# Optimization experiments

Hardware: AMD Instinct MI355X
Metric: run time of the kernel (lower is better)

The kernel has to match this reference:

```python
import jax, jax.numpy as jnp
import numpy as np

INPUT_DIM = 1024
HIDDEN_DIM = 1024

def setup_inputs() -> dict:
    key = jax.random.key(0)
    ks = jax.random.split(key, 9)
    s_in = 1.0 / np.sqrt(INPUT_DIM)
    s_h = 1.0 / np.sqrt(HIDDEN_DIM)
    x = jax.random.normal(ks[0], (4, 2048, INPUT_DIM), dtype=jnp.float32)
    Wq = jax.random.uniform(ks[1], (INPUT_DIM, HIDDEN_DIM), jnp.float32, -s_in, s_in)
    bq = jax.random.uniform(ks[2], (HIDDEN_DIM,), jnp.float32, -s_in, s_in)
    Wk = jax.random.uniform(ks[3], (INPUT_DIM, HIDDEN_DIM), jnp.float32, -s_in, s_in)
    bk = jax.random.uniform(ks[4], (HIDDEN_DIM,), jnp.float32, -s_in, s_in)
    Wv = jax.random.uniform(ks[5], (INPUT_DIM, HIDDEN_DIM), jnp.float32, -s_in, s_in)
    bv = jax.random.uniform(ks[6], (HIDDEN_DIM,), jnp.float32, -s_in, s_in)
    Wo = jax.random.uniform(ks[7], (HIDDEN_DIM, INPUT_DIM), jnp.float32, -s_h, s_h)
    bo = jax.random.uniform(ks[8], (INPUT_DIM,), jnp.float32, -s_h, s_h)
    return {"x": x, "Wq": Wq, "bq": bq, "Wk": Wk, "bk": bk, "Wv": Wv, "bv": bv, "Wo": Wo, "bo": bo}

def reference(x, Wq, bq, Wk, bk, Wv, bv, Wo, bo):
    # x: [B, S, D_in]; scale uses x.shape[-1] (faithful to source, which divides by sqrt(input_dim))
    scale = 1.0 / jnp.sqrt(jnp.asarray(x.shape[-1], dtype=x.dtype))
    Q = jnp.einsum('bsd,dh->bsh', x, Wq) + bq
    K = jnp.einsum('bsd,dh->bsh', x, Wk) + bk
    V = jnp.einsum('bsd,dh->bsh', x, Wv) + bv
    scores = jnp.einsum('bqh,bkh->bqk', Q, K) * scale  # [B, S, S]
    attn = jax.nn.softmax(scores, axis=-1)
    ctx = jnp.einsum('bqk,bkh->bqh', attn, V)
    return jnp.einsum('bsh,hd->bsd', ctx, Wo) + bo
```

## Files before the change

kernel.cpp:

```cpp
#include <hip/hip_runtime.h>

typedef __attribute__((ext_vector_type(8))) short bf16x8;
typedef __attribute__((ext_vector_type(4))) float f32x4;
typedef __attribute__((ext_vector_type(4))) unsigned short us4;

#define AS1 __attribute__((address_space(1)))
#define AS3 __attribute__((address_space(3)))

__device__ __forceinline__ unsigned short f2bf(float f) {
  unsigned u = __float_as_uint(f);
  u += 0x7fff + ((u >> 16) & 1);
  return (unsigned short)(u >> 16);
}

__device__ __forceinline__ void gload_lds16(const void* g, void* l) {
  __builtin_amdgcn_global_load_lds((const AS1 unsigned int*)g,
                                   (AS3 unsigned int*)l, 16, 0, 0);
}

#define MFMA16(a, b, c) __builtin_amdgcn_mfma_f32_16x16x32_bf16(a, b, c, 0, 0, 0)

template <typename OutT, bool BIAS, int MODE>
__global__ __launch_bounds__(512, 2) void gemm8p(
    const unsigned short* __restrict__ A,
    const unsigned short* __restrict__ Bt,
    OutT* __restrict__ C,
    unsigned short* __restrict__ Vt,
    const float* __restrict__ bias,
    int Kd, int lda, int ldb, int ldc,
    long sA, long sB, long sC,
    float scale) {
  constexpr int BOFF = 256 * 64;
  __shared__ unsigned short lds[2][512 * 64];

  const int bz = blockIdx.z;
  A  += (size_t)bz * sA + (size_t)blockIdx.x * 256 * lda;
  Bt += (size_t)bz * sB + (size_t)blockIdx.y * 256 * ldb;

  const int tid  = threadIdx.x;
  const int wave = tid >> 6;
  const int lane = tid & 63;
  const int wm   = wave >> 2;
  const int wn   = wave & 3;
  const int l15  = lane & 15;
  const int hi   = lane >> 4;
  const int sr  = (wave << 3) + (lane >> 3);
  const int sc8 = lane & 7;
  const int co0 = ((hi    ) ^ (lane & 7)) << 3;
  const int co1 = ((hi + 4) ^ (lane & 7)) << 3;
  const int rA0 = wm * 128 + l15;
  const int rB0 = wn * 32 + l15;

  auto stA = [&](int b, int k0, int r0) {
    const unsigned short* g =
        A + (size_t)(r0 + sr) * lda + (k0 + ((sc8 ^ (sr & 7)) << 3));
    gload_lds16(g, &lds[b][(r0 + (wave << 3)) * 64]);
  };
  auto stB = [&](int b, int k0, int r0) {
    const int lr = r0 + sr;
    const int gr = ((lr >> 5) & 3) * 64 + ((lr >> 7) << 5) + (lr & 31);
    const unsigned short* g =
        Bt + (size_t)gr * ldb + (k0 + ((sc8 ^ (lr & 7)) << 3));
    gload_lds16(g, &lds[b][BOFF + (r0 + (wave << 3)) * 64]);
  };

  f32x4 acc[8][4] = {};
  bf16x8 af[4][2], b0f[2][2], b1f[2][2];

  stA(0, 0, 0);   stA(0, 0, 128);
  stB(0, 0, 0);   stB(0, 0, 64);
  stB(0, 0, 128); stB(0, 0, 192);
  stA(0, 0, 64);  stA(0, 0, 192);
  asm volatile("s_waitcnt vmcnt(4)" ::: "memory");
  __builtin_amdgcn_s_barrier();

  const int NT = Kd >> 6;
  for (int t = 0; t < NT; ++t) {
    const int buf = t & 1;
    const int nb  = buf ^ 1;
    const int nk0 = (t + 1) << 6;
    const bool st = (t + 1) < NT;
    const unsigned short* Lr = &lds[buf][0];

#pragma unroll
    for (int mt = 0; mt < 4; ++mt) {
      af[mt][0] = *(const bf16x8*)&Lr[(rA0 + mt * 16) * 64 + co0];
      af[mt][1] = *(const bf16x8*)&Lr[(rA0 + mt * 16) * 64 + co1];
    }
#pragma unroll
    for (int n = 0; n < 2; ++n) {
      b0f[n][0] = *(const bf16x8*)&Lr[BOFF + (rB0 + n * 16) * 64 + co0];
      b0f[n][1] = *(const bf16x8*)&Lr[BOFF + (rB0 + n * 16) * 64 + co1];
    }
    if (st) { stA(nb, nk0, 0); stA(nb, nk0, 128); stB(nb, nk0, 0); stB(nb, nk0, 64); }
    __builtin_amdgcn_s_barrier();
    __builtin_amdgcn_s_setprio(1);
#pragma unroll
    for (int mt = 0; mt < 4; ++mt)
#pragma unroll
      for (int n = 0; n < 2; ++n) {
        acc[mt][n] = MFMA16(af[mt][0], b0f[n][0], acc[mt][n]);
        acc[mt][n] = MFMA16(af[mt][1], b0f[n][1], acc[mt][n]);
      }
    __builtin_amdgcn_s_setprio(0);
    if (st) asm volatile("s_waitcnt vmcnt(4)" ::: "memory");
    else    asm volatile("s_waitcnt vmcnt(0)" ::: "memory");
    __builtin_amdgcn_s_barrier();

#pragma unroll
    for (int n = 0; n < 2; ++n) {
      b1f[n][0] = *(const bf16x8*)&Lr[BOFF + (128 + rB0 + n * 16) * 64 + co0];
      b1f[n][1] = *(const bf16x8*)&Lr[BOFF + (128 + rB0 + n * 16) * 64 + co1];
    }
    if (st) { stB(nb, nk0, 128); stB(nb, nk0, 192); stA(nb, nk0, 64); stA(nb, nk0, 192); }
    __builtin_amdgcn_s_barrier();
    __builtin_amdgcn_s_setprio(1);
#pragma unroll
    for (int mt = 0; mt < 4; ++mt)
#pragma unroll
      for (int n = 0; n < 2; ++n) {
        acc[mt][2 + n] = MFMA16(af[mt][0], b1f[n][0], acc[mt][2 + n]);
        acc[mt][2 + n] = MFMA16(af[mt][1], b1f[n][1], acc[mt][2 + n]);
      }
    __builtin_amdgcn_s_setprio(0);
    __builtin_amdgcn_s_barrier();

#pragma unroll
    for (int mt = 0; mt < 4; ++mt) {
      af[mt][0] = *(const bf16x8*)&Lr[(64 + rA0 + mt * 16) * 64 + co0];
      af[mt][1] = *(const bf16x8*)&Lr[(64 + rA0 + mt * 16) * 64 + co1];
    }
    __builtin_amdgcn_s_barrier();
    __builtin_amdgcn_s_setprio(1);
#pragma unroll
    for (int mt = 0; mt < 4; ++mt)
#pragma unroll
      for (int n = 0; n < 2; ++n) {
        acc[4 + mt][2 + n] = MFMA16(af[mt][0], b1f[n][0], acc[4 + mt][2 + n]);
        acc[4 + mt][2 + n] = MFMA16(af[mt][1], b1f[n][1], acc[4 + mt][2 + n]);
      }
    __builtin_amdgcn_s_setprio(0);
    __builtin_amdgcn_s_barrier();

    __builtin_amdgcn_s_barrier();
    __builtin_amdgcn_s_setprio(1);
#pragma unroll
    for (int mt = 0; mt < 4; ++mt)
#pragma unroll
      for (int n = 0; n < 2; ++n) {
        acc[4 + mt][n] = MFMA16(af[mt][0], b0f[n][0], acc[4 + mt][n]);
        acc[4 + mt][n] = MFMA16(af[mt][1], b0f[n][1], acc[4 + mt][n]);
      }
    __builtin_amdgcn_s_setprio(0);
    if (st) asm volatile("s_waitcnt vmcnt(4)" ::: "memory");
    __builtin_amdgcn_s_barrier();
  }

  const int hi4  = hi << 2;
  const int row0 = blockIdx.x * 256 + wm * 128;
  const int col0 = blockIdx.y * 256 + wn * 64;

  if constexpr (MODE == 1) {
    const int piece = col0 >> 10;
    float bvv[4];
#pragma unroll
    for (int nt = 0; nt < 4; ++nt)
      bvv[nt] = BIAS ? bias[col0 + nt * 16 + l15] : 0.0f;
    if (piece < 2) {
      OutT* dst = C + (size_t)piece * sC;
      const int cb = (col0 & 1023) + l15;
#pragma unroll
      for (int mt = 0; mt < 8; ++mt)
#pragma unroll
        for (int r = 0; r < 4; ++r) {
          const size_t rowoff = (size_t)(row0 + mt * 16 + hi4 + r) * ldc;
#pragma unroll
          for (int nt = 0; nt < 4; ++nt)
            dst[rowoff + cb + nt * 16] = (OutT)f2bf(acc[mt][nt][r] * scale + bvv[nt]);
        }
    } else {
      const int b = blockIdx.x >> 3;
      const int sb = (blockIdx.x & 7) * 256 + wm * 128 + hi4;
#pragma unroll
      for (int nt = 0; nt < 4; ++nt) {
        const int d = ((col0 + nt * 16) & 1023) + l15;
#pragma unroll
        for (int mt = 0; mt < 8; ++mt) {
          us4 pk;
          pk.x = f2bf(acc[mt][nt][0] * scale + bvv[nt]);
          pk.y = f2bf(acc[mt][nt][1] * scale + bvv[nt]);
          pk.z = f2bf(acc[mt][nt][2] * scale + bvv[nt]);
          pk.w = f2bf(acc[mt][nt][3] * scale + bvv[nt]);
          *(us4*)&Vt[((size_t)b << 21) + (size_t)d * 2048 + sb + mt * 16] = pk;
        }
      }
    }
  } else {
    C += (size_t)bz * sC;
    float bvv[4];
#pragma unroll
    for (int nt = 0; nt < 4; ++nt)
      bvv[nt] = BIAS ? bias[col0 + nt * 16 + l15] : 0.0f;
    const int cb = col0 + l15;
#pragma unroll
    for (int mt = 0; mt < 8; ++mt)
#pragma unroll
      for (int r = 0; r < 4; ++r) {
        const size_t rowoff = (size_t)(row0 + mt * 16 + hi4 + r) * ldc;
#pragma unroll
        for (int nt = 0; nt < 4; ++nt) {
          const float v = acc[mt][nt][r] * scale + bvv[nt];
          if constexpr (sizeof(OutT) == 4)
            C[rowoff + cb + nt * 16] = v;
          else
            C[rowoff + cb + nt * 16] = (OutT)f2bf(v);
        }
      }
  }
}

__global__ void cvt_x(const float* __restrict__ in, unsigned short* __restrict__ out, int n4) {
  const int i = blockIdx.x * blockDim.x + threadIdx.x;
  if (i < n4) {
    const float4 v = ((const float4*)in)[i];
    uint2 o;
    o.x = (unsigned)f2bf(v.x) | ((unsigned)f2bf(v.y) << 16);
    o.y = (unsigned)f2bf(v.z) | ((unsigned)f2bf(v.w) << 16);
    ((uint2*)out)[i] = o;
  }
}

__global__ void cvtT_w4(const float* __restrict__ Wq, const float* __restrict__ Wk,
                        const float* __restrict__ Wv, const float* __restrict__ Wo,
                        unsigned short* __restrict__ Wqkvb, unsigned short* __restrict__ Wob) {
  __shared__ unsigned short tile[64][65];
  const int z = blockIdx.z;
  const float* in = (z == 0) ? Wq : (z == 1) ? Wk : (z == 2) ? Wv : Wo;
  unsigned short* out = (z == 3) ? Wob : Wqkvb + (size_t)z * 1024 * 1024;
  const int r0 = blockIdx.y * 64, c0 = blockIdx.x * 64;
  for (int i = threadIdx.y; i < 64; i += 4)
    tile[i][threadIdx.x] = f2bf(in[(size_t)(r0 + i) * 1024 + c0 + threadIdx.x]);
  __syncthreads();
  for (int i = threadIdx.y; i < 64; i += 4)
    out[(size_t)(c0 + i) * 1024 + r0 + threadIdx.x] = tile[threadIdx.x][i];
}

__global__ void concat_bias(const float* __restrict__ bq, const float* __restrict__ bk,
                            const float* __restrict__ bv, float* __restrict__ dst) {
  const int z = blockIdx.x;
  const float* src = (z == 0) ? bq : (z == 1) ? bk : bv;
  const int i = threadIdx.x;
  ((float4*)(dst + z * 1024))[i] = ((const float4*)src)[i];
}

__global__ __launch_bounds__(256) void softmax_bf16(unsigned short* __restrict__ scores) {
  unsigned short* p = scores + (size_t)blockIdx.x * 2048;
  const int t = threadIdx.x;
  uint4 raw = ((const uint4*)p)[t];
  float v[8];
  v[0] = __uint_as_float(raw.x << 16); v[1] = __uint_as_float(raw.x & 0xffff0000u);
  v[2] = __uint_as_float(raw.y << 16); v[3] = __uint_as_float(raw.y & 0xffff0000u);
  v[4] = __uint_as_float(raw.z << 16); v[5] = __uint_as_float(raw.z & 0xffff0000u);
  v[6] = __uint_as_float(raw.w << 16); v[7] = __uint_as_float(raw.w & 0xffff0000u);

  float m = v[0];
#pragma unroll
  for (int i = 1; i < 8; ++i) m = fmaxf(m, v[i]);
#pragma unroll
  for (int off = 32; off; off >>= 1) m = fmaxf(m, __shfl_xor(m, off, 64));

  __shared__ float red[4];
  __shared__ float bcast[2];
  const int wave = t >> 6, lane = t & 63;
  if (lane == 0) red[wave] = m;
  __syncthreads();
  if (t == 0) bcast[0] = fmaxf(fmaxf(red[0], red[1]), fmaxf(red[2], red[3]));
  __syncthreads();
  m = bcast[0];

  float s = 0.f;
#pragma unroll
  for (int i = 0; i < 8; ++i) { v[i] = __expf(v[i] - m); s += v[i]; }
#pragma unroll
  for (int off = 32; off; off >>= 1) s += __shfl_xor(s, off, 64);
  if (lane == 0) red[wave] = s;
  __syncthreads();
  if (t == 0) bcast[1] = red[0] + red[1] + red[2] + red[3];
  __syncthreads();
  const float inv = 1.0f / bcast[1];

  uint4 ov;
  ov.x = (unsigned)f2bf(v[0] * inv) | ((unsigned)f2bf(v[1] * inv) << 16);
  ov.y = (unsigned)f2bf(v[2] * inv) | ((unsigned)f2bf(v[3] * inv) << 16);
  ov.z = (unsigned)f2bf(v[4] * inv) | ((unsigned)f2bf(v[5] * inv) << 16);
  ov.w = (unsigned)f2bf(v[6] * inv) | ((unsigned)f2bf(v[7] * inv) << 16);
  ((uint4*)p)[t] = ov;
}

extern "C" void kernel_launch(void* const* d_in, const int* in_sizes, int n_in,
                              void* d_out, int out_size, void* d_ws, size_t ws_size,
                              hipStream_t stream) {
  const float* x  = (const float*)d_in[0];
  const float* Wq = (const float*)d_in[1];
  const float* bq = (const float*)d_in[2];
  const float* Wk = (const float*)d_in[3];
  const float* bk = (const float*)d_in[4];
  const float* Wv = (const float*)d_in[5];
  const float* bv = (const float*)d_in[6];
  const float* Wo = (const float*)d_in[7];
  const float* bo = (const float*)d_in[8];
  float* out = (float*)d_out;

  char* ws = (char*)d_ws;
  size_t off = 0;
  auto alloc = [&](size_t bytes) { char* p = ws + off; off += (bytes + 255) & ~255UL; return p; };
  unsigned short* xb    = (unsigned short*)alloc(8192UL * 1024 * 2);
  unsigned short* Wqkvb = (unsigned short*)alloc(3072UL * 1024 * 2);
  unsigned short* Wob   = (unsigned short*)alloc(1024UL * 1024 * 2);
  float*          bqkv  = (float*)alloc(3072UL * 4);
  unsigned short* Qb    = (unsigned short*)alloc(8192UL * 1024 * 2);
  unsigned short* Kb    = (unsigned short*)alloc(8192UL * 1024 * 2);
  unsigned short* Vtb   = (unsigned short*)alloc(4UL * 1024 * 2048 * 2);
  unsigned short* attn  = (unsigned short*)alloc(8192UL * 2048 * 2);
  unsigned short* ctxb  = (unsigned short*)alloc(8192UL * 1024 * 2);

  const dim3 blk(512);

  cvt_x<<<2097152 / 256, 256, 0, stream>>>(x, xb, 2097152);
  cvtT_w4<<<dim3(16, 16, 4), dim3(64, 4), 0, stream>>>(Wq, Wk, Wv, Wo, Wqkvb, Wob);
  concat_bias<<<3, 256, 0, stream>>>(bq, bk, bv, bqkv);

  gemm8p<unsigned short, true, 1><<<dim3(32, 12, 1), blk, 0, stream>>>(
      xb, Wqkvb, Qb, Vtb, bqkv, 1024, 1024, 1024, 1024, 0, 0, 8192L * 1024, 1.0f);

  gemm8p<unsigned short, false, 0><<<dim3(8, 8, 4), blk, 0, stream>>>(
      Qb, Kb, attn, nullptr, nullptr, 1024, 1024, 1024, 2048,
      2048L * 1024, 2048L * 1024, 2048L * 2048, 0.03125f);

  softmax_bf16<<<8192, 256, 0, stream>>>(attn);

  gemm8p<unsigned short, false, 0><<<dim3(8, 4, 4), blk, 0, stream>>>(
      attn, Vtb, ctxb, nullptr, nullptr, 2048, 2048, 2048, 1024,
      2048L * 2048, 1024L * 2048, 2048L * 1024, 1.0f);

  gemm8p<float, true, 0><<<dim3(32, 4, 1), blk, 0, stream>>>(
      ctxb, Wob, out, nullptr, bo, 1024, 1024, 1024, 1024, 0, 0, 0, 1.0f);
}
```

Before: 323.4 us.

## Replace 256x256 ping-pong GEMM with 256x128 triple-buffered K=32 pipeline

Rewrites the shared GEMM kernel to use 256x128 output tiles with K-steps of 32 and a three-stage LDS ring buffer, replacing the 256x256, K=64 double-buffered schedule with its interleaved barriers. Each wave now computes a 64x64 subtile with one barrier per K-step, and the grids double along N to match. This aims to simplify synchronisation, raise block count and occupancy, and hide load latency with a deeper prefetch. In exchange each tile gets less operand reuse, and the XOR swizzle is dropped from the LDS layout, which may cause LDS bank conflicts.

```diff
diff --git a/kernel.cpp b/kernel.cpp
--- a/kernel.cpp
+++ b/kernel.cpp
@@ -21,7 +21,7 @@
 #define MFMA16(a, b, c) __builtin_amdgcn_mfma_f32_16x16x32_bf16(a, b, c, 0, 0, 0)
 
 template <typename OutT, bool BIAS, int MODE>
-__global__ __launch_bounds__(512, 2) void gemm8p(
+__global__ __launch_bounds__(512, 2) void gemmk(
     const unsigned short* __restrict__ A,
     const unsigned short* __restrict__ Bt,
     OutT* __restrict__ C,
@@ -30,135 +30,72 @@
     int Kd, int lda, int ldb, int ldc,
     long sA, long sB, long sC,
     float scale) {
-  constexpr int BOFF = 256 * 64;
-  __shared__ unsigned short lds[2][512 * 64];
+  constexpr int ABUF  = 256 * 32;
+  constexpr int BUFSZ = ABUF + 128 * 32;
+  __shared__ unsigned short lds[3 * BUFSZ];
 
   const int bz = blockIdx.z;
   A  += (size_t)bz * sA + (size_t)blockIdx.x * 256 * lda;
-  Bt += (size_t)bz * sB + (size_t)blockIdx.y * 256 * ldb;
+  Bt += (size_t)bz * sB + (size_t)blockIdx.y * 128 * ldb;
 
   const int tid  = threadIdx.x;
   const int wave = tid >> 6;
   const int lane = tid & 63;
-  const int wm   = wave >> 2;
-  const int wn   = wave & 3;
+  const int wm   = wave >> 1;
+  const int wn   = wave & 1;
   const int l15  = lane & 15;
   const int hi   = lane >> 4;
-  const int sr  = (wave << 3) + (lane >> 3);
-  const int sc8 = lane & 7;
-  const int co0 = ((hi    ) ^ (lane & 7)) << 3;
-  const int co1 = ((hi + 4) ^ (lane & 7)) << 3;
-  const int rA0 = wm * 128 + l15;
-  const int rB0 = wn * 32 + l15;
-
-  auto stA = [&](int b, int k0, int r0) {
-    const unsigned short* g =
-        A + (size_t)(r0 + sr) * lda + (k0 + ((sc8 ^ (sr & 7)) << 3));
-    gload_lds16(g, &lds[b][(r0 + (wave << 3)) * 64]);
+  const int srow = tid >> 2;
+  const int schk = (tid & 3) * 8;
+
+  auto stage = [&](int bi, int k0) {
+    unsigned short* L = &lds[bi * BUFSZ + wave * 512];
+    const unsigned short* ga = A + (size_t)srow * lda + (k0 + schk);
+    gload_lds16(ga, L);
+    gload_lds16(ga + (size_t)128 * lda, L + 4096);
+    gload_lds16(Bt + (size_t)srow * ldb + (k0 + schk), L + 8192);
   };
-  auto stB = [&](int b, int k0, int r0) {
-    const int lr = r0 + sr;
-    const int gr = ((lr >> 5) & 3) * 64 + ((lr >> 7) << 5) + (lr & 31);
-    const unsigned short* g =
-        Bt + (size_t)gr * ldb + (k0 + ((sc8 ^ (lr & 7)) << 3));
-    gload_lds16(g, &lds[b][BOFF + (r0 + (wave << 3)) * 64]);
-  };
-
-  f32x4 acc[8][4] = {};
-  bf16x8 af[4][2], b0f[2][2], b1f[2][2];
-
-  stA(0, 0, 0);   stA(0, 0, 128);
-  stB(0, 0, 0);   stB(0, 0, 64);
-  stB(0, 0, 128); stB(0, 0, 192);
-  stA(0, 0, 64);  stA(0, 0, 192);
-  asm volatile("s_waitcnt vmcnt(4)" ::: "memory");
+
+  f32x4 acc[4][4] = {};
+
+  stage(0, 0);
+  stage(1, 32);
+  asm volatile("s_waitcnt vmcnt(3)" ::: "memory");
   __builtin_amdgcn_s_barrier();
 
-  const int NT = Kd >> 6;
+  const int NT = Kd >> 5;
+  int bufi = 0;
+  const int rdA = (wm * 64 + l15) * 32 + hi * 8;
+  const int rdB = ABUF + (wn * 64 + l15) * 32 + hi * 8;
   for (int t = 0; t < NT; ++t) {
-    const int buf = t & 1;
-    const int nb  = buf ^ 1;
-    const int nk0 = (t + 1) << 6;
-    const bool st = (t + 1) < NT;
-    const unsigned short* Lr = &lds[buf][0];
-
-#pragma unroll
-    for (int mt = 0; mt < 4; ++mt) {
-      af[mt][0] = *(const bf16x8*)&Lr[(rA0 + mt * 16) * 64 + co0];
-      af[mt][1] = *(const bf16x8*)&Lr[(rA0 + mt * 16) * 64 + co1];
+    if (t + 2 < NT) {
+      int nbi = bufi + 2; if (nbi >= 3) nbi -= 3;
+      stage(nbi, (t + 2) << 5);
     }
-#pragma unroll
-    for (int n = 0; n < 2; ++n) {
-      b0f[n][0] = *(const bf16x8*)&Lr[BOFF + (rB0 + n * 16) * 64 + co0];
-      b0f[n][1] = *(const bf16x8*)&Lr[BOFF + (rB0 + n * 16) * 64 + co1];
-    }
-    if (st) { stA(nb, nk0, 0); stA(nb, nk0, 128); stB(nb, nk0, 0); stB(nb, nk0, 64); }
+    const unsigned short* L = &lds[bufi * BUFSZ];
+    bf16x8 af[4], bf[4];
+#pragma unroll
+    for (int mt = 0; mt < 4; ++mt)
+      af[mt] = *(const bf16x8*)&L[rdA + mt * 16 * 32];
+#pragma unroll
+    for (int nt = 0; nt < 4; ++nt)
+      bf[nt] = *(const bf16x8*)&L[rdB + nt * 16 * 32];
+    __builtin_amdgcn_s_setprio(1);
+#pragma unroll
+    for (int mt = 0; mt < 4; ++mt)
+#pragma unroll
+      for (int nt = 0; nt < 4; ++nt)
+        acc[mt][nt] = MFMA16(af[mt], bf[nt], acc[mt][nt]);
+    __builtin_amdgcn_s_setprio(0);
+    if (t + 2 < NT)      asm volatile("s_waitcnt vmcnt(3)" ::: "memory");
+    else if (t + 1 < NT) asm volatile("s_waitcnt vmcnt(0)" ::: "memory");
     __builtin_amdgcn_s_barrier();
-    __builtin_amdgcn_s_setprio(1);
-#pragma unroll
-    for (int mt = 0; mt < 4; ++mt)
-#pragma unroll
-      for (int n = 0; n < 2; ++n) {
-        acc[mt][n] = MFMA16(af[mt][0], b0f[n][0], acc[mt][n]);
-        acc[mt][n] = MFMA16(af[mt][1], b0f[n][1], acc[mt][n]);
-      }
-    __builtin_amdgcn_s_setprio(0);
-    if (st) asm volatile("s_waitcnt vmcnt(4)" ::: "memory");
-    else    asm volatile("s_waitcnt vmcnt(0)" ::: "memory");
-    __builtin_amdgcn_s_barrier();
-
-#pragma unroll
-    for (int n = 0; n < 2; ++n) {
-      b1f[n][0] = *(const bf16x8*)&Lr[BOFF + (128 + rB0 + n * 16) * 64 + co0];
-      b1f[n][1] = *(const bf16x8*)&Lr[BOFF + (128 + rB0 + n * 16) * 64 + co1];
-    }
-    if (st) { stB(nb, nk0, 128); stB(nb, nk0, 192); stA(nb, nk0, 64); stA(nb, nk0, 192); }
-    __builtin_amdgcn_s_barrier();
-    __builtin_amdgcn_s_setprio(1);
-#pragma unroll
-    for (int mt = 0; mt < 4; ++mt)
-#pragma unroll
-      for (int n = 0; n < 2; ++n) {
-        acc[mt][2 + n] = MFMA16(af[mt][0], b1f[n][0], acc[mt][2 + n]);
-        acc[mt][2 + n] = MFMA16(af[mt][1], b1f[n][1], acc[mt][2 + n]);
-      }
-    __builtin_amdgcn_s_setprio(0);
-    __builtin_amdgcn_s_barrier();
-
-#pragma unroll
-    for (int mt = 0; mt < 4; ++mt) {
-      af[mt][0] = *(const bf16x8*)&Lr[(64 + rA0 + mt * 16) * 64 + co0];
-      af[mt][1] = *(const bf16x8*)&Lr[(64 + rA0 + mt * 16) * 64 + co1];
-    }
-    __builtin_amdgcn_s_barrier();
-    __builtin_amdgcn_s_setprio(1);
-#pragma unroll
-    for (int mt = 0; mt < 4; ++mt)
-#pragma unroll
-      for (int n = 0; n < 2; ++n) {
-        acc[4 + mt][2 + n] = MFMA16(af[mt][0], b1f[n][0], acc[4 + mt][2 + n]);
-        acc[4 + mt][2 + n] = MFMA16(af[mt][1], b1f[n][1], acc[4 + mt][2 + n]);
-      }
-    __builtin_amdgcn_s_setprio(0);
-    __builtin_amdgcn_s_barrier();
-
-    __builtin_amdgcn_s_barrier();
-    __builtin_amdgcn_s_setprio(1);
-#pragma unroll
-    for (int mt = 0; mt < 4; ++mt)
-#pragma unroll
-      for (int n = 0; n < 2; ++n) {
-        acc[4 + mt][n] = MFMA16(af[mt][0], b0f[n][0], acc[4 + mt][n]);
-        acc[4 + mt][n] = MFMA16(af[mt][1], b0f[n][1], acc[4 + mt][n]);
-      }
-    __builtin_amdgcn_s_setprio(0);
-    if (st) asm volatile("s_waitcnt vmcnt(4)" ::: "memory");
-    __builtin_amdgcn_s_barrier();
+    bufi = (bufi + 1 == 3) ? 0 : bufi + 1;
   }
 
   const int hi4  = hi << 2;
-  const int row0 = blockIdx.x * 256 + wm * 128;
-  const int col0 = blockIdx.y * 256 + wn * 64;
+  const int row0 = blockIdx.x * 256 + wm * 64;
+  const int col0 = blockIdx.y * 128 + wn * 64;
 
   if constexpr (MODE == 1) {
     const int piece = col0 >> 10;
@@ -170,7 +107,7 @@
       OutT* dst = C + (size_t)piece * sC;
       const int cb = (col0 & 1023) + l15;
 #pragma unroll
-      for (int mt = 0; mt < 8; ++mt)
+      for (int mt = 0; mt < 4; ++mt)
 #pragma unroll
         for (int r = 0; r < 4; ++r) {
           const size_t rowoff = (size_t)(row0 + mt * 16 + hi4 + r) * ldc;
@@ -180,12 +117,12 @@
         }
     } else {
       const int b = blockIdx.x >> 3;
-      const int sb = (blockIdx.x & 7) * 256 + wm * 128 + hi4;
+      const int sb = (blockIdx.x & 7) * 256 + wm * 64 + hi4;
 #pragma unroll
       for (int nt = 0; nt < 4; ++nt) {
         const int d = ((col0 + nt * 16) & 1023) + l15;
 #pragma unroll
-        for (int mt = 0; mt < 8; ++mt) {
+        for (int mt = 0; mt < 4; ++mt) {
           us4 pk;
           pk.x = f2bf(acc[mt][nt][0] * scale + bvv[nt]);
           pk.y = f2bf(acc[mt][nt][1] * scale + bvv[nt]);
@@ -203,7 +140,7 @@
       bvv[nt] = BIAS ? bias[col0 + nt * 16 + l15] : 0.0f;
     const int cb = col0 + l15;
 #pragma unroll
-    for (int mt = 0; mt < 8; ++mt)
+    for (int mt = 0; mt < 4; ++mt)
 #pragma unroll
       for (int r = 0; r < 4; ++r) {
         const size_t rowoff = (size_t)(row0 + mt * 16 + hi4 + r) * ldc;
@@ -330,19 +267,19 @@
   cvtT_w4<<<dim3(16, 16, 4), dim3(64, 4), 0, stream>>>(Wq, Wk, Wv, Wo, Wqkvb, Wob);
   concat_bias<<<3, 256, 0, stream>>>(bq, bk, bv, bqkv);
 
-  gemm8p<unsigned short, true, 1><<<dim3(32, 12, 1), blk, 0, stream>>>(
+  gemmk<unsigned short, true, 1><<<dim3(32, 24, 1), blk, 0, stream>>>(
       xb, Wqkvb, Qb, Vtb, bqkv, 1024, 1024, 1024, 1024, 0, 0, 8192L * 1024, 1.0f);
 
-  gemm8p<unsigned short, false, 0><<<dim3(8, 8, 4), blk, 0, stream>>>(
+  gemmk<unsigned short, false, 0><<<dim3(8, 16, 4), blk, 0, stream>>>(
       Qb, Kb, attn, nullptr, nullptr, 1024, 1024, 1024, 2048,
       2048L * 1024, 2048L * 1024, 2048L * 2048, 0.03125f);
 
   softmax_bf16<<<8192, 256, 0, stream>>>(attn);
 
-  gemm8p<unsigned short, false, 0><<<dim3(8, 4, 4), blk, 0, stream>>>(
+  gemmk<unsigned short, false, 0><<<dim3(8, 8, 4), blk, 0, stream>>>(
       attn, Vtb, ctxb, nullptr, nullptr, 2048, 2048, 2048, 1024,
       2048L * 2048, 1024L * 2048, 2048L * 1024, 1.0f);
 
-  gemm8p<float, true, 0><<<dim3(32, 4, 1), blk, 0, stream>>>(
+  gemmk<float, true, 0><<<dim3(32, 8, 1), blk, 0, stream>>>(
       ctxb, Wob, out, nullptr, bo, 1024, 1024, 1024, 1024, 0, 0, 0, 1.0f);
 }
```

Result: faster. 298.2 us (-7.8%).
